# Kernel tuning notes

Hardware: AMD Instinct MI355X
Metric: run time of the kernel (lower is better)

The kernel has to match this reference:

```python
import jax, jax.numpy as jnp
import numpy as np

N = 100000
E = 800000
IN = 64
HID = 32
H1 = 4
G = 256  # num graphs
OUT = 1
NEG_SLOPE = 0.2


def setup_inputs() -> dict:
    key = jax.random.key(0)
    ks = jax.random.split(key, 16)
    x = jax.random.normal(ks[0], (N, IN), dtype=jnp.float32)
    edge_index = jax.random.randint(ks[1], (2, E), 0, N, dtype=jnp.int64)
    batch = jnp.sort(jax.random.randint(ks[2], (N,), 0, G, dtype=jnp.int64))

    def xavier(k, shape):
        fan_in, fan_out = shape[0], shape[1]
        lim = float(np.sqrt(6.0 / (fan_in + fan_out)))
        return jax.random.uniform(k, shape, jnp.float32, -lim, lim)

    # GATv2 layer 1: in=IN, out=HID, heads=H1
    Wl1 = xavier(ks[3], (IN, H1 * HID)); bl1 = jnp.zeros((H1 * HID,), jnp.float32)
    Wr1 = xavier(ks[4], (IN, H1 * HID)); br1 = jnp.zeros((H1 * HID,), jnp.float32)
    att1 = xavier(ks[5], (H1, HID))
    bias1 = jnp.zeros((H1 * HID,), jnp.float32)
    # GATv2 layer 2: in=H1*HID, out=HID, heads=1
    Wl2 = xavier(ks[6], (H1 * HID, HID)); bl2 = jnp.zeros((HID,), jnp.float32)
    Wr2 = xavier(ks[7], (H1 * HID, HID)); br2 = jnp.zeros((HID,), jnp.float32)
    att2 = xavier(ks[8], (1, HID))
    bias2 = jnp.zeros((HID,), jnp.float32)
    # head MLP
    Wh1 = xavier(ks[9], (HID, HID)); bh1 = jnp.zeros((HID,), jnp.float32)
    Wh2 = xavier(ks[10], (HID, OUT)); bh2 = jnp.zeros((OUT,), jnp.float32)
    return dict(x=x, edge_index=edge_index, batch=batch,
                Wl1=Wl1, bl1=bl1, Wr1=Wr1, br1=br1, att1=att1, bias1=bias1,
                Wl2=Wl2, bl2=bl2, Wr2=Wr2, br2=br2, att2=att2, bias2=bias2,
                Wh1=Wh1, bh1=bh1, Wh2=Wh2, bh2=bh2)


def gatv2_conv(x, src, dst, Wl, bl, Wr, br, att, bias, heads, out_ch):
    n = x.shape[0]
    xl = (x @ Wl + bl).reshape(n, heads, out_ch)  # source transform (x_j)
    xr = (x @ Wr + br).reshape(n, heads, out_ch)  # target transform (x_i)
    e = jax.nn.leaky_relu(xl[src] + xr[dst], NEG_SLOPE)        # [E,H,C]
    alpha = jnp.einsum('ehc,hc->eh', e, att)                    # [E,H]
    amax = jax.ops.segment_max(alpha, dst, num_segments=n)      # [N,H]
    ea = jnp.exp(alpha - amax[dst])
    denom = jax.ops.segment_sum(ea, dst, num_segments=n)
    a = ea / (denom[dst] + 1e-16)                               # softmax per dst node
    out = jax.ops.segment_sum(xl[src] * a[:, :, None], dst, num_segments=n)
    return out.reshape(n, heads * out_ch) + bias


def reference(x, edge_index, batch,
              Wl1, bl1, Wr1, br1, att1, bias1,
              Wl2, bl2, Wr2, br2, att2, bias2,
              Wh1, bh1, Wh2, bh2):
    n = x.shape[0]
    # add self-loops (PyG GATv2Conv default)
    loops = jnp.arange(n, dtype=edge_index.dtype)
    src = jnp.concatenate([edge_index[0], loops])
    dst = jnp.concatenate([edge_index[1], loops])

    h = gatv2_conv(x, src, dst, Wl1, bl1, Wr1, br1, att1, bias1, H1, HID)
    h = jax.nn.celu(h, alpha=1.0)
    # dropout: identity in eval mode
    h = gatv2_conv(h, src, dst, Wl2, bl2, Wr2, br2, att2, bias2, 1, HID)

    # global mean pool over graphs
    sums = jax.ops.segment_sum(h, batch, num_segments=G)          # [G,HID]
    counts = jax.ops.segment_sum(jnp.ones((n,), h.dtype), batch, num_segments=G)
    pooled = sums / jnp.maximum(counts, 1.0)[:, None]

    z = jax.nn.relu(pooled @ Wh1 + bh1)
    return z @ Wh2 + bh2  # [G, OUT]
```

## Files before the change

kernel.cpp:

```cpp
#include <hip/hip_runtime.h>
#include <hip/hip_fp16.h>
#include <math.h>

#define NN 100000
#define NE 800000
#define ET (NN + NE)
#define NG 256
#define SLOPE 0.2f
#define LOG2E 1.44269504088896340736f
#define NB1 ((NN + 255) / 256)
#define NRT 6250

typedef _Float16 f16x2 __attribute__((ext_vector_type(2)));
typedef _Float16 f16x8 __attribute__((ext_vector_type(8)));
typedef float    f32x4 __attribute__((ext_vector_type(4)));

__device__ __forceinline__ void unpack8(float4 raw, float* x) {
    const __half2* hp = (const __half2*)&raw;
    #pragma unroll
    for (int j = 0; j < 4; ++j) {
        float2 f = __half22float2(hp[j]);
        x[2 * j] = f.x; x[2 * j + 1] = f.y;
    }
}
__device__ __forceinline__ void unpack4(float2 raw, float* x) {
    const __half2* hp = (const __half2*)&raw;
    #pragma unroll
    for (int j = 0; j < 2; ++j) {
        float2 f = __half22float2(hp[j]);
        x[2 * j] = f.x; x[2 * j + 1] = f.y;
    }
}

template<int K, int MT, int MHALF>
__global__ void packW_kernel(const float* __restrict__ Wl, const float* __restrict__ Wr,
                             __half* __restrict__ hi, __half* __restrict__ lo)
{
    constexpr int KS  = K / 32;
    constexpr int TOT = (MT / 16) * KS * 64 * 8;
    for (int idx = blockIdx.x * 256 + threadIdx.x; idx < TOT; idx += gridDim.x * 256) {
        const int i   = idx & 7;
        const int l   = (idx >> 3) & 63;
        const int rem = idx >> 9;
        const int ks  = rem % KS;
        const int ct  = rem / KS;
        const int k   = ks * 32 + (l >> 4) * 8 + i;
        const int col = ct * 16 + (l & 15);
        const float w = (col < MHALF) ? Wl[(size_t)k * MHALF + col]
                                      : Wr[(size_t)k * MHALF + (col - MHALF)];
        const __half h = __float2half(w);
        hi[idx] = h;
        lo[idx] = __float2half(w - __half2float(h));
    }
}

__global__ __launch_bounds__(256, 4)
void t1_mfma_kernel(const float* __restrict__ X,
                    const __half* __restrict__ Whi, const __half* __restrict__ Wlo,
                    const float* __restrict__ bl, const float* __restrict__ br,
                    __half* __restrict__ XLh, __half* __restrict__ XRh)
{
    const int rt = blockIdx.x * 4 + (threadIdx.x >> 6);
    if (rt >= NRT) return;
    const int l = threadIdx.x & 63;
    const int row_a = rt * 16 + (l & 15);
    const int kbase = (l >> 4) * 8;

    f16x8 a[2];
    #pragma unroll
    for (int ks = 0; ks < 2; ++ks) {
        const float4 x0 = *(const float4*)(X + (size_t)row_a * 64 + ks * 32 + kbase);
        const float4 x1 = *(const float4*)(X + (size_t)row_a * 64 + ks * 32 + kbase + 4);
        a[ks][0] = (_Float16)x0.x; a[ks][1] = (_Float16)x0.y;
        a[ks][2] = (_Float16)x0.z; a[ks][3] = (_Float16)x0.w;
        a[ks][4] = (_Float16)x1.x; a[ks][5] = (_Float16)x1.y;
        a[ks][6] = (_Float16)x1.z; a[ks][7] = (_Float16)x1.w;
    }

    for (int ct = 0; ct < 16; ++ct) {
        f32x4 acc = {0.f, 0.f, 0.f, 0.f};
        #pragma unroll
        for (int ks = 0; ks < 2; ++ks) {
            const f16x8 bh = *(const f16x8*)(Whi + ((size_t)(ct * 2 + ks) * 64 + l) * 8);
            const f16x8 bL = *(const f16x8*)(Wlo + ((size_t)(ct * 2 + ks) * 64 + l) * 8);
            acc = __builtin_amdgcn_mfma_f32_16x16x32_f16(a[ks], bh, acc, 0, 0, 0);
            acc = __builtin_amdgcn_mfma_f32_16x16x32_f16(a[ks], bL, acc, 0, 0, 0);
        }
        const int col = ct * 16 + (l & 15);
        const float bias = (col < 128) ? bl[col] : br[col - 128];
        __half* const dst = (col < 128) ? XLh : XRh;
        const int dcol = col & 127;
        #pragma unroll
        for (int r = 0; r < 4; ++r) {
            const int row = rt * 16 + (l >> 4) * 4 + r;
            dst[(size_t)row * 128 + dcol] = __float2half(acc[r] + bias);
        }
    }
}

__global__ __launch_bounds__(256, 4)
void t2_mfma_kernel(const __half* __restrict__ H1h,
                    const __half* __restrict__ Whi, const __half* __restrict__ Wlo,
                    const float* __restrict__ bl, const float* __restrict__ br,
                    __half* __restrict__ XLh, __half* __restrict__ XRh)
{
    const int rt = blockIdx.x * 4 + (threadIdx.x >> 6);
    if (rt >= NRT) return;
    const int l = threadIdx.x & 63;
    const int row_a = rt * 16 + (l & 15);
    const int kbase = (l >> 4) * 8;

    f16x8 a[4];
    #pragma unroll
    for (int ks = 0; ks < 4; ++ks)
        a[ks] = *(const f16x8*)(H1h + (size_t)row_a * 128 + ks * 32 + kbase);

    for (int ct = 0; ct < 4; ++ct) {
        f32x4 acc = {0.f, 0.f, 0.f, 0.f};
        #pragma unroll
        for (int ks = 0; ks < 4; ++ks) {
            const f16x8 bh = *(const f16x8*)(Whi + ((size_t)(ct * 4 + ks) * 64 + l) * 8);
            const f16x8 bL = *(const f16x8*)(Wlo + ((size_t)(ct * 4 + ks) * 64 + l) * 8);
            acc = __builtin_amdgcn_mfma_f32_16x16x32_f16(a[ks], bh, acc, 0, 0, 0);
            acc = __builtin_amdgcn_mfma_f32_16x16x32_f16(a[ks], bL, acc, 0, 0, 0);
        }
        const int col = ct * 16 + (l & 15);
        const float bias = (col < 32) ? bl[col] : br[col - 32];
        __half* const dst = (col < 32) ? XLh : XRh;
        const int dcol = col & 31;
        #pragma unroll
        for (int r = 0; r < 4; ++r) {
            const int row = rt * 16 + (l >> 4) * 4 + r;
            dst[(size_t)row * 32 + dcol] = __float2half(acc[r] + bias);
        }
    }
}

__global__ void hist_kernel(const int* __restrict__ edst, int* __restrict__ deg)
{
    int e = blockIdx.x * 256 + threadIdx.x;
    if (e >= ET) return;
    int d = (e < NE) ? edst[e] : (e - NE);
    atomicAdd(deg + d, 1);
}

__global__ void scan1_kernel(const int* __restrict__ deg, int* __restrict__ rowstart,
                             int* __restrict__ bsum)
{
    __shared__ int lds[256];
    int t = threadIdx.x, idx = blockIdx.x * 256 + t;
    int v = (idx < NN) ? deg[idx] : 0;
    lds[t] = v;
    __syncthreads();
    #pragma unroll
    for (int off = 1; off < 256; off <<= 1) {
        int add = (t >= off) ? lds[t - off] : 0;
        __syncthreads();
        lds[t] += add;
        __syncthreads();
    }
    if (idx < NN) rowstart[idx + 1] = lds[t];
    if (t == 255) bsum[blockIdx.x] = lds[255];
}

__global__ void scan2_kernel(int* __restrict__ bsum)
{
    __shared__ int lds[512];
    int t = threadIdx.x;
    int v = (t < NB1) ? bsum[t] : 0;
    lds[t] = v;
    __syncthreads();
    #pragma unroll
    for (int off = 1; off < 512; off <<= 1) {
        int add = (t >= off) ? lds[t - off] : 0;
        __syncthreads();
        lds[t] += add;
        __syncthreads();
    }
    if (t < NB1) bsum[t] = lds[t] - v;
}

__global__ void scan3_kernel(int* __restrict__ rowstart, const int* __restrict__ bsum)
{
    int idx = blockIdx.x * 256 + threadIdx.x;
    if (idx == 0) rowstart[0] = 0;
    if (idx < NN) rowstart[idx + 1] += bsum[blockIdx.x];
}

__global__ void scatter_kernel(const int* __restrict__ esrc, const int* __restrict__ edst,
                               const int* __restrict__ rowstart,
                               int* __restrict__ cursor, int* __restrict__ csr_src)
{
    int e = blockIdx.x * 256 + threadIdx.x;
    if (e >= ET) return;
    int s, d;
    if (e < NE) { s = esrc[e]; d = edst[e]; } else { s = e - NE; d = s; }
    int pos = rowstart[d] + atomicAdd(cursor + d, 1);
    csr_src[pos] = s;
}

__global__ void gat1_kernel(const int* __restrict__ rowstart, const int* __restrict__ csr_src,
                            const __half* __restrict__ XLh, const __half* __restrict__ XRh,
                            const float* __restrict__ att, const float* __restrict__ bias,
                            __half* __restrict__ H1h)
{
    const int node = blockIdx.x * 4 + (threadIdx.x >> 6);
    if (node >= NN) return;
    const int lane = threadIdx.x & 63;
    const int slot = lane >> 4;
    const int q    = lane & 15;
    const int c0   = q * 8;

    float4 xr_raw = *(const float4*)(XRh + (size_t)node * 128 + c0);
    const f16x2* xrh = (const f16x2*)&xr_raw;
    f16x2 ath[4];
    {
        const float4 a0 = *(const float4*)(att + c0);
        const float4 a1 = *(const float4*)(att + c0 + 4);
        ath[0] = (f16x2){(_Float16)(a0.x * LOG2E), (_Float16)(a0.y * LOG2E)};
        ath[1] = (f16x2){(_Float16)(a0.z * LOG2E), (_Float16)(a0.w * LOG2E)};
        ath[2] = (f16x2){(_Float16)(a1.x * LOG2E), (_Float16)(a1.y * LOG2E)};
        ath[3] = (f16x2){(_Float16)(a1.z * LOG2E), (_Float16)(a1.w * LOG2E)};
    }
    const f16x2 s2 = {(_Float16)SLOPE, (_Float16)SLOPE};
    const int beg = rowstart[node], end = rowstart[node + 1];
    float m = -INFINITY, ssum = 0.f;
    float acc[8] = {0.f, 0.f, 0.f, 0.f, 0.f, 0.f, 0.f, 0.f};

    bool valid = (beg + slot) < end;
    int s = valid ? csr_src[beg + slot] : 0;
    float4 cur = *(const float4*)(XLh + (size_t)s * 128 + c0);

    for (int i = beg; i < end; i += 4) {
        const int nidx    = i + 4 + slot;
        const bool nvalid = nidx < end;
        const int ns      = nvalid ? csr_src[nidx] : 0;
        const float4 nxt  = *(const float4*)(XLh + (size_t)ns * 128 + c0);

        const f16x2* xlh = (const f16x2*)&cur;
        float p = 0.f;
        #pragma unroll
        for (int j = 0; j < 4; ++j) {
            f16x2 v  = xlh[j] + xrh[j];
            f16x2 lv = __builtin_elementwise_max(v, s2 * v);
            p = __builtin_amdgcn_fdot2(lv, ath[j], p, false);
        }
        p += __shfl_xor(p, 1);
        p += __shfl_xor(p, 2);
        if (!valid) p = -INFINITY;
        float pm = fmaxf(p, __shfl_xor(p, 16));
        pm = fmaxf(pm, __shfl_xor(pm, 32));
        if (__any(pm > m + 8.f)) {
            const float mn = fmaxf(m, pm);
            const float sc = exp2f(m - mn);
            ssum *= sc;
            #pragma unroll
            for (int j = 0; j < 8; ++j) acc[j] *= sc;
            m = mn;
        }
        const float e = exp2f(p - m);
        ssum += e;
        float xlf[8];
        unpack8(cur, xlf);
        #pragma unroll
        for (int j = 0; j < 8; ++j)
            acc[j] = fmaf(e, xlf[j], acc[j]);

        cur = nxt;
        valid = nvalid;
    }
    ssum += __shfl_xor(ssum, 16);
    ssum += __shfl_xor(ssum, 32);
    #pragma unroll
    for (int j = 0; j < 8; ++j) {
        acc[j] += __shfl_xor(acc[j], 16);
        acc[j] += __shfl_xor(acc[j], 32);
    }
    if (slot == 0) {
        const float inv = 1.f / (ssum + 1e-16f);
        const float4 b0 = *(const float4*)(bias + c0);
        const float4 b1 = *(const float4*)(bias + c0 + 4);
        const float bb[8] = {b0.x, b0.y, b0.z, b0.w, b1.x, b1.y, b1.z, b1.w};
        __half2 outh[4];
        #pragma unroll
        for (int j = 0; j < 4; ++j) {
            float o0 = acc[2 * j] * inv + bb[2 * j];
            float o1 = acc[2 * j + 1] * inv + bb[2 * j + 1];
            o0 = o0 > 0.f ? o0 : expm1f(o0);
            o1 = o1 > 0.f ? o1 : expm1f(o1);
            outh[j] = __float22half2_rn(make_float2(o0, o1));
        }
        *(float4*)(H1h + (size_t)node * 128 + c0) = *(const float4*)outh;
    }
}

__global__ void gat2_kernel(const int* __restrict__ rowstart, const int* __restrict__ csr_src,
                            const __half* __restrict__ XLh, const __half* __restrict__ XRh,
                            const float* __restrict__ att,
                            float* __restrict__ H2)
{
    const int node = blockIdx.x * 8 + (threadIdx.x >> 5);
    if (node >= NN) return;
    const int l2   = threadIdx.x & 31;
    const int slot = l2 >> 3;
    const int q    = l2 & 7;
    const int c0   = q * 4;

    float2 xr_raw = *(const float2*)(XRh + (size_t)node * 32 + c0);
    const f16x2* xrh = (const f16x2*)&xr_raw;
    f16x2 ath[2];
    {
        const float4 a = *(const float4*)(att + c0);
        ath[0] = (f16x2){(_Float16)(a.x * LOG2E), (_Float16)(a.y * LOG2E)};
        ath[1] = (f16x2){(_Float16)(a.z * LOG2E), (_Float16)(a.w * LOG2E)};
    }
    const f16x2 s2 = {(_Float16)SLOPE, (_Float16)SLOPE};
    const int beg = rowstart[node], end = rowstart[node + 1];
    float m = -INFINITY, ssum = 0.f;
    float acc[4] = {0.f, 0.f, 0.f, 0.f};

    bool valid = (beg + slot) < end;
    int s = valid ? csr_src[beg + slot] : 0;
    float2 cur = *(const float2*)(XLh + (size_t)s * 32 + c0);

    for (int i = beg; i < end; i += 4) {
        const int nidx    = i + 4 + slot;
        const bool nvalid = nidx < end;
        const int ns      = nvalid ? csr_src[nidx] : 0;
        const float2 nxt  = *(const float2*)(XLh + (size_t)ns * 32 + c0);

        const f16x2* xlh = (const f16x2*)&cur;
        float p = 0.f;
        #pragma unroll
        for (int j = 0; j < 2; ++j) {
            f16x2 v  = xlh[j] + xrh[j];
            f16x2 lv = __builtin_elementwise_max(v, s2 * v);
            p = __builtin_amdgcn_fdot2(lv, ath[j], p, false);
        }
        p += __shfl_xor(p, 1);
        p += __shfl_xor(p, 2);
        p += __shfl_xor(p, 4);
        if (!valid) p = -INFINITY;
        float pm = fmaxf(p, __shfl_xor(p, 8));
        pm = fmaxf(pm, __shfl_xor(pm, 16));
        if (__any(pm > m + 8.f)) {
            const float mn = fmaxf(m, pm);
            const float sc = exp2f(m - mn);
            ssum *= sc;
            #pragma unroll
            for (int j = 0; j < 4; ++j) acc[j] *= sc;
            m = mn;
        }
        const float e = exp2f(p - m);
        ssum += e;
        float xlf[4];
        unpack4(cur, xlf);
        #pragma unroll
        for (int j = 0; j < 4; ++j)
            acc[j] = fmaf(e, xlf[j], acc[j]);

        cur = nxt;
        valid = nvalid;
    }
    ssum += __shfl_xor(ssum, 8);
    ssum += __shfl_xor(ssum, 16);
    #pragma unroll
    for (int j = 0; j < 4; ++j) {
        acc[j] += __shfl_xor(acc[j], 8);
        acc[j] += __shfl_xor(acc[j], 16);
    }
    if (slot == 0) {
        const float inv = 1.f / (ssum + 1e-16f);
        float4 o;
        o.x = acc[0] * inv; o.y = acc[1] * inv;
        o.z = acc[2] * inv; o.w = acc[3] * inv;
        *(float4*)(H2 + (size_t)node * 32 + c0) = o;
    }
}

__global__ void pool_kernel(const float* __restrict__ h2, const float* __restrict__ bias2,
                            const int* __restrict__ batch,
                            float* __restrict__ pool, float* __restrict__ cnt)
{
    const int c    = threadIdx.x & 31;
    const int slot = threadIdx.x >> 5;
    const int base = blockIdx.x * 256;
    const float b = bias2[c];
    float acc = 0.f, cacc = 0.f;
    int curg = -1;
    for (int i = slot; i < 256; i += 8) {
        int node = base + i;
        if (node >= NN) break;
        int g = batch[node];
        if (g != curg) {
            if (curg >= 0) {
                atomicAdd(pool + (size_t)curg * 32 + c, acc);
                if (c == 0) atomicAdd(cnt + curg, cacc);
            }
            acc = 0.f; cacc = 0.f; curg = g;
        }
        acc += h2[(size_t)node * 32 + c] + b;
        cacc += 1.f;
    }
    if (curg >= 0) {
        atomicAdd(pool + (size_t)curg * 32 + c, acc);
        if (c == 0) atomicAdd(cnt + curg, cacc);
    }
}

__global__ void head_kernel(const float* __restrict__ pool, const float* __restrict__ cnt,
                            const float* __restrict__ Wh1, const float* __restrict__ bh1,
                            const float* __restrict__ Wh2, const float* __restrict__ bh2,
                            float* __restrict__ out)
{
    int g = blockIdx.x;
    int c = threadIdx.x;
    float partial = 0.f;
    if (c < 32) {
        float invc = 1.f / fmaxf(cnt[g], 1.f);
        float acc = bh1[c];
        #pragma unroll
        for (int k = 0; k < 32; ++k)
            acc = fmaf(pool[g * 32 + k] * invc, Wh1[k * 32 + c], acc);
        float z = fmaxf(acc, 0.f);
        partial = z * Wh2[c];
    }
    #pragma unroll
    for (int off = 32; off >= 1; off >>= 1)
        partial += __shfl_down(partial, off);
    if (c == 0) out[g] = partial + bh2[0];
}

extern "C" void kernel_launch(void* const* d_in, const int* in_sizes, int n_in,
                              void* d_out, int out_size, void* d_ws, size_t ws_size,
                              hipStream_t stream)
{
    const float* x     = (const float*)d_in[0];
    const int*   ei    = (const int*)d_in[1];
    const int*   batch = (const int*)d_in[2];
    const float* Wl1   = (const float*)d_in[3];
    const float* bl1   = (const float*)d_in[4];
    const float* Wr1   = (const float*)d_in[5];
    const float* br1   = (const float*)d_in[6];
    const float* att1  = (const float*)d_in[7];
    const float* bias1 = (const float*)d_in[8];
    const float* Wl2   = (const float*)d_in[9];
    const float* bl2   = (const float*)d_in[10];
    const float* Wr2   = (const float*)d_in[11];
    const float* br2   = (const float*)d_in[12];
    const float* att2  = (const float*)d_in[13];
    const float* bias2 = (const float*)d_in[14];
    const float* Wh1   = (const float*)d_in[15];
    const float* bh1   = (const float*)d_in[16];
    const float* Wh2   = (const float*)d_in[17];
    const float* bh2   = (const float*)d_in[18];
    const int* esrc = ei;
    const int* edst = ei + NE;

    char* wsb = (char*)d_ws;
    __half* xl1h = (__half*)wsb;
    __half* xr1h = (__half*)(wsb + (size_t)NN * 128 * 2);
    __half* h1h  = xr1h;
    char* p2 = wsb + (size_t)NN * 128 * 4;
    __half* xl2h = (__half*)p2;
    __half* xr2h = (__half*)(p2 + (size_t)NN * 32 * 2);
    float*  h2   = (float*)(p2 + (size_t)NN * 32 * 4);
    int*    zr     = (int*)(p2 + (size_t)NN * 32 * 8);
    int*    deg    = zr;
    int*    cursor = zr + NN;
    float*  pool   = (float*)(zr + 2 * NN);
    float*  cnt    = pool + (size_t)NG * 32;
    int* rowstart  = (int*)(cnt + NG);
    int* bsum      = rowstart + NN + 1;
    int* csr_src   = bsum + 512;
    __half* whi1   = (__half*)(csr_src + ET);
    __half* wlo1   = whi1 + 16384;
    __half* whi2   = wlo1 + 16384;
    __half* wlo2   = whi2 + 8192;

    hipMemsetAsync(zr, 0, (size_t)(2 * NN + NG * 32 + NG) * sizeof(int), stream);
    packW_kernel<64, 256, 128><<<64, 256, 0, stream>>>(Wl1, Wr1, whi1, wlo1);
    packW_kernel<128, 64, 32><<<32, 256, 0, stream>>>(Wl2, Wr2, whi2, wlo2);
    hist_kernel<<<(ET + 255) / 256, 256, 0, stream>>>(edst, deg);
    scan1_kernel<<<NB1, 256, 0, stream>>>(deg, rowstart, bsum);
    scan2_kernel<<<1, 512, 0, stream>>>(bsum);
    scan3_kernel<<<NB1, 256, 0, stream>>>(rowstart, bsum);
    scatter_kernel<<<(ET + 255) / 256, 256, 0, stream>>>(esrc, edst, rowstart, cursor, csr_src);

    t1_mfma_kernel<<<(NRT + 3) / 4, 256, 0, stream>>>(
        x, whi1, wlo1, bl1, br1, xl1h, xr1h);
    gat1_kernel<<<(NN + 3) / 4, 256, 0, stream>>>(
        rowstart, csr_src, xl1h, xr1h, att1, bias1, h1h);

    t2_mfma_kernel<<<(NRT + 3) / 4, 256, 0, stream>>>(
        h1h, whi2, wlo2, bl2, br2, xl2h, xr2h);
    gat2_kernel<<<(NN + 7) / 8, 256, 0, stream>>>(
        rowstart, csr_src, xl2h, xr2h, att2, h2);

    pool_kernel<<<(NN + 255) / 256, 256, 0, stream>>>(h2, bias2, batch, pool, cnt);
    head_kernel<<<NG, 64, 0, stream>>>(pool, cnt, Wh1, bh1, Wh2, bh2, (float*)d_out);
}
```

Measured before the change: 262.4 us.

## Fuse weight packing with degree histogram and fold pooling into gat2

```diff
diff --git a/kernel.cpp b/kernel.cpp
--- a/kernel.cpp
+++ b/kernel.cpp
@@ -10,6 +10,7 @@
 #define LOG2E 1.44269504088896340736f
 #define NB1 ((NN + 255) / 256)
 #define NRT 6250
+#define NBH ((ET + 255) / 256)
 
 typedef _Float16 f16x2 __attribute__((ext_vector_type(2)));
 typedef _Float16 f16x8 __attribute__((ext_vector_type(8)));
@@ -32,25 +33,44 @@
     }
 }
 
-template<int K, int MT, int MHALF>
-__global__ void packW_kernel(const float* __restrict__ Wl, const float* __restrict__ Wr,
-                             __half* __restrict__ hi, __half* __restrict__ lo)
-{
-    constexpr int KS  = K / 32;
-    constexpr int TOT = (MT / 16) * KS * 64 * 8;
-    for (int idx = blockIdx.x * 256 + threadIdx.x; idx < TOT; idx += gridDim.x * 256) {
-        const int i   = idx & 7;
-        const int l   = (idx >> 3) & 63;
-        const int rem = idx >> 9;
-        const int ks  = rem % KS;
-        const int ct  = rem / KS;
-        const int k   = ks * 32 + (l >> 4) * 8 + i;
-        const int col = ct * 16 + (l & 15);
-        const float w = (col < MHALF) ? Wl[(size_t)k * MHALF + col]
-                                      : Wr[(size_t)k * MHALF + (col - MHALF)];
-        const __half h = __float2half(w);
-        hi[idx] = h;
-        lo[idx] = __float2half(w - __half2float(h));
+template<int K, int MHALF>
+__device__ __forceinline__ void packW_body(int idx,
+                                           const float* __restrict__ Wl,
+                                           const float* __restrict__ Wr,
+                                           __half* __restrict__ hi, __half* __restrict__ lo)
+{
+    constexpr int KS = K / 32;
+    const int i   = idx & 7;
+    const int l   = (idx >> 3) & 63;
+    const int rem = idx >> 9;
+    const int ks  = rem % KS;
+    const int ct  = rem / KS;
+    const int k   = ks * 32 + (l >> 4) * 8 + i;
+    const int col = ct * 16 + (l & 15);
+    const float w = (col < MHALF) ? Wl[(size_t)k * MHALF + col]
+                                  : Wr[(size_t)k * MHALF + (col - MHALF)];
+    const __half h = __float2half(w);
+    hi[idx] = h;
+    lo[idx] = __float2half(w - __half2float(h));
+}
+
+__global__ void init_kernel(const float* __restrict__ Wl1, const float* __restrict__ Wr1,
+                            __half* __restrict__ whi1, __half* __restrict__ wlo1,
+                            const float* __restrict__ Wl2, const float* __restrict__ Wr2,
+                            __half* __restrict__ whi2, __half* __restrict__ wlo2,
+                            const int* __restrict__ edst, int* __restrict__ deg)
+{
+    const int b = blockIdx.x;
+    if (b < 64) {
+        packW_body<64, 128>(b * 256 + threadIdx.x, Wl1, Wr1, whi1, wlo1);
+    } else if (b < 96) {
+        packW_body<128, 32>((b - 64) * 256 + threadIdx.x, Wl2, Wr2, whi2, wlo2);
+    } else {
+        const int e = (b - 96) * 256 + threadIdx.x;
+        if (e < ET) {
+            int d = (e < NE) ? edst[e] : (e - NE);
+            atomicAdd(deg + d, 1);
+        }
     }
 }
 
@@ -134,14 +154,6 @@
             dst[(size_t)row * 32 + dcol] = __float2half(acc[r] + bias);
         }
     }
-}
-
-__global__ void hist_kernel(const int* __restrict__ edst, int* __restrict__ deg)
-{
-    int e = blockIdx.x * 256 + threadIdx.x;
-    if (e >= ET) return;
-    int d = (e < NE) ? edst[e] : (e - NE);
-    atomicAdd(deg + d, 1);
 }
 
 __global__ void scan1_kernel(const int* __restrict__ deg, int* __restrict__ rowstart,
@@ -296,8 +308,9 @@
 
 __global__ void gat2_kernel(const int* __restrict__ rowstart, const int* __restrict__ csr_src,
                             const __half* __restrict__ XLh, const __half* __restrict__ XRh,
-                            const float* __restrict__ att,
-                            float* __restrict__ H2)
+                            const float* __restrict__ att, const float* __restrict__ bias2,
+                            const int* __restrict__ batch,
+                            float* __restrict__ pool, float* __restrict__ cnt)
 {
     const int node = blockIdx.x * 8 + (threadIdx.x >> 5);
     if (node >= NN) return;
@@ -371,40 +384,11 @@
     }
     if (slot == 0) {
         const float inv = 1.f / (ssum + 1e-16f);
-        float4 o;
-        o.x = acc[0] * inv; o.y = acc[1] * inv;
-        o.z = acc[2] * inv; o.w = acc[3] * inv;
-        *(float4*)(H2 + (size_t)node * 32 + c0) = o;
-    }
-}
-
-__global__ void pool_kernel(const float* __restrict__ h2, const float* __restrict__ bias2,
-                            const int* __restrict__ batch,
-                            float* __restrict__ pool, float* __restrict__ cnt)
-{
-    const int c    = threadIdx.x & 31;
-    const int slot = threadIdx.x >> 5;
-    const int base = blockIdx.x * 256;
-    const float b = bias2[c];
-    float acc = 0.f, cacc = 0.f;
-    int curg = -1;
-    for (int i = slot; i < 256; i += 8) {
-        int node = base + i;
-        if (node >= NN) break;
-        int g = batch[node];
-        if (g != curg) {
-            if (curg >= 0) {
-                atomicAdd(pool + (size_t)curg * 32 + c, acc);
-                if (c == 0) atomicAdd(cnt + curg, cacc);
-            }
-            acc = 0.f; cacc = 0.f; curg = g;
-        }
-        acc += h2[(size_t)node * 32 + c] + b;
-        cacc += 1.f;
-    }
-    if (curg >= 0) {
-        atomicAdd(pool + (size_t)curg * 32 + c, acc);
-        if (c == 0) atomicAdd(cnt + curg, cacc);
+        const int g = batch[node];
+        #pragma unroll
+        for (int j = 0; j < 4; ++j)
+            atomicAdd(pool + (size_t)g * 32 + c0 + j, acc[j] * inv + bias2[c0 + j]);
+        if (q == 0) atomicAdd(cnt + g, 1.f);
     }
 }
 
@@ -464,8 +448,7 @@
     char* p2 = wsb + (size_t)NN * 128 * 4;
     __half* xl2h = (__half*)p2;
     __half* xr2h = (__half*)(p2 + (size_t)NN * 32 * 2);
-    float*  h2   = (float*)(p2 + (size_t)NN * 32 * 4);
-    int*    zr     = (int*)(p2 + (size_t)NN * 32 * 8);
+    int*    zr     = (int*)(p2 + (size_t)NN * 32 * 4);
     int*    deg    = zr;
     int*    cursor = zr + NN;
     float*  pool   = (float*)(zr + 2 * NN);
@@ -479,9 +462,8 @@
     __half* wlo2   = whi2 + 8192;
 
     hipMemsetAsync(zr, 0, (size_t)(2 * NN + NG * 32 + NG) * sizeof(int), stream);
-    packW_kernel<64, 256, 128><<<64, 256, 0, stream>>>(Wl1, Wr1, whi1, wlo1);
-    packW_kernel<128, 64, 32><<<32, 256, 0, stream>>>(Wl2, Wr2, whi2, wlo2);
-    hist_kernel<<<(ET + 255) / 256, 256, 0, stream>>>(edst, deg);
+    init_kernel<<<96 + NBH, 256, 0, stream>>>(Wl1, Wr1, whi1, wlo1,
+                                              Wl2, Wr2, whi2, wlo2, edst, deg);
     scan1_kernel<<<NB1, 256, 0, stream>>>(deg, rowstart, bsum);
     scan2_kernel<<<1, 512, 0, stream>>>(bsum);
     scan3_kernel<<<NB1, 256, 0, stream>>>(rowstart, bsum);
@@ -495,8 +477,7 @@
     t2_mfma_kernel<<<(NRT + 3) / 4, 256, 0, stream>>>(
         h1h, whi2, wlo2, bl2, br2, xl2h, xr2h);
     gat2_kernel<<<(NN + 7) / 8, 256, 0, stream>>>(
-        rowstart, csr_src, xl2h, xr2h, att2, h2);
-
-    pool_kernel<<<(NN + 255) / 256, 256, 0, stream>>>(h2, bias2, batch, pool, cnt);
+        rowstart, csr_src, xl2h, xr2h, att2, bias2, batch, pool, cnt);
+
     head_kernel<<<NG, 64, 0, stream>>>(pool, cnt, Wh1, bh1, Wh2, bh2, (float*)d_out);
 }
```

Result: slower. 525.8 us (+100.4%).
